# Kernel tuning notes

Measured on AMD Instinct MI355X. Metric: run time of the kernel, lower is better.

Reference implementation:

```python
import jax, jax.numpy as jnp
import numpy as np

B, C, W = 32768, 142, 10
K, D = 4096, 128
EPS = 1e-5


def _ln(x, g, b):
    m = jnp.mean(x, axis=-1, keepdims=True)
    v = jnp.var(x, axis=-1, keepdims=True)
    return (x - m) * jax.lax.rsqrt(v + EPS) * g + b


def setup_inputs() -> dict:
    key = jax.random.key(0)
    ks = jax.random.split(key, 10)
    s = lambda fi, fo: (2.0 / (fi + fo)) ** 0.5
    return {
        "x": jax.random.normal(ks[0], (B, C, W), jnp.float32),
        "W1": jax.random.normal(ks[1], (1420, 512), jnp.float32) * s(1420, 512),
        "b1": jnp.zeros((512,), jnp.float32),
        "g1": jnp.ones((512,), jnp.float32),
        "be1": jnp.zeros((512,), jnp.float32),
        "W2": jax.random.normal(ks[2], (512, 256), jnp.float32) * s(512, 256),
        "b2": jnp.zeros((256,), jnp.float32),
        "g2": jnp.ones((256,), jnp.float32),
        "be2": jnp.zeros((256,), jnp.float32),
        "W3": jax.random.normal(ks[3], (256, D), jnp.float32) * s(256, D),
        "b3": jnp.zeros((D,), jnp.float32),
        "emb": jax.random.normal(ks[4], (K, D), jnp.float32),
        "W4": jax.random.normal(ks[5], (D, 256), jnp.float32) * s(D, 256),
        "b4": jnp.zeros((256,), jnp.float32),
        "g3": jnp.ones((256,), jnp.float32),
        "be3": jnp.zeros((256,), jnp.float32),
        "W5": jax.random.normal(ks[6], (256, 128), jnp.float32) * s(256, 128),
        "b5": jnp.zeros((128,), jnp.float32),
        "W6": jax.random.normal(ks[7], (128, 2), jnp.float32) * s(128, 2),
        "b6": jnp.zeros((2,), jnp.float32),
    }


def reference(x, W1, b1, g1, be1, W2, b2, g2, be2, W3, b3, emb,
              W4, b4, g3, be3, W5, b5, W6, b6):
    # ----- encoder (eval mode: dropout is identity) -----
    xf = x.reshape(x.shape[0], -1)                      # [B, 1420]
    h = jax.nn.gelu(_ln(xf @ W1 + b1, g1, be1), approximate=False)
    h = jax.nn.gelu(_ln(h @ W2 + b2, g2, be2), approximate=False)
    z_e = h @ W3 + b3                                   # [B, D]

    # ----- EMA VQ (eval: no buffer updates) -----
    # squared distances give the same argmin as torch.cdist
    d2 = (jnp.sum(z_e * z_e, axis=-1, keepdims=True)
          - 2.0 * (z_e @ emb.T)
          + jnp.sum(emb * emb, axis=-1))                # [B, K]
    indices = jnp.argmin(d2, axis=-1)                   # [B] int
    z_q = emb[indices]                                  # [B, D]

    commitment_loss = 0.25 * jnp.mean((jax.lax.stop_gradient(z_q) - z_e) ** 2)
    z_q_st = z_e + jax.lax.stop_gradient(z_q - z_e)     # straight-through

    # histogram instead of materializing [B, K] one-hot
    counts = jnp.zeros((K,), jnp.float32).at[indices].add(1.0)
    avg_probs = counts / x.shape[0]
    perplexity = jnp.exp(-jnp.sum(avg_probs * jnp.log(avg_probs + 1e-10)))
    n_active = jnp.sum(avg_probs > 0.001)

    # ----- decoder (eval mode) -----
    d = jax.nn.gelu(_ln(z_q_st @ W4 + b4, g3, be3), approximate=False)
    d = jax.nn.gelu(d @ W5 + b5, approximate=False)
    velocity_pred = d @ W6 + b6                         # [B, 2]

    return (velocity_pred, z_e, z_q_st, indices, commitment_loss,
            perplexity, n_active)
```

## Files before the change

### kernel.cpp

```cpp
#include <hip/hip_runtime.h>

#define B_ROWS 32768
#define KCODES 4096

typedef float f32x4 __attribute__((ext_vector_type(4)));
typedef _Float16 f16x8 __attribute__((ext_vector_type(8)));
typedef _Float16 f16x4 __attribute__((ext_vector_type(4)));

struct Split { _Float16 h, m; };

__device__ __forceinline__ Split split2(float v)
{
  Split s;
  s.h = (_Float16)v;
  s.m = (_Float16)((v - (float)s.h) * 256.f);
  return s;
}

template<bool SPLITA>
__global__ __launch_bounds__(256, 3)
void hgemm(const float* __restrict__ Af, const _Float16* __restrict__ Ah,
           const _Float16* __restrict__ Am, int Astr,
           const _Float16* __restrict__ Bh, const _Float16* __restrict__ Bm,
           const float* __restrict__ bias, float* __restrict__ C,
           int M, int N, int K, int Kp, int nbx)
{
  __shared__ _Float16 As1[128 * 40];
  __shared__ _Float16 As2[128 * 40];
  __shared__ _Float16 Bs1[64 * 40];
  __shared__ _Float16 Bs2[64 * 40];

  const int flat = blockIdx.x;
  const int s_   = flat >> 3;
  const int mb   = (s_ / nbx) * 8 + (flat & 7);
  const int nb   = s_ % nbx;
  const int m0   = mb * 128;
  const int n0   = nb * 64;

  const int tid  = threadIdx.x;
  const int lane = tid & 63;
  const int wid  = tid >> 6;
  const int l15  = lane & 15;
  const int lg   = lane >> 4;
  const int wm   = (wid >> 1) * 64;
  const int wn   = (wid & 1) * 32;

  f32x4 hi[4][2], mid[4][2];
  #pragma unroll
  for (int i = 0; i < 4; ++i)
    #pragma unroll
    for (int j = 0; j < 2; ++j) { hi[i][j] = (f32x4)0.f; mid[i][j] = (f32x4)0.f; }

  const int sar = tid >> 1;
  const int sak = (tid & 1) << 4;
  const int far = tid >> 2;
  const int fak = (tid & 3) << 3;
  const int sbn = tid >> 2;
  const int sbk = (tid & 3) << 3;

  const int nk = Kp >> 5;
  #pragma unroll 1
  for (int kt = 0; kt < nk; ++kt) {
    const int k0 = kt << 5;
    if (SPLITA) {
      #pragma unroll
      for (int p = 0; p < 2; ++p) {
        const int r = far + (p << 6);
        const int c = k0 + fak;
        const float* src = Af + (size_t)(m0 + r) * K + c;
        float4 v0 = make_float4(0.f, 0.f, 0.f, 0.f), v1 = v0;
        if (c < K)     v0 = *reinterpret_cast<const float4*>(src);
        if (c + 4 < K) v1 = *reinterpret_cast<const float4*>(src + 4);
        const Split s0 = split2(v0.x), s1 = split2(v0.y), s2 = split2(v0.z), s3 = split2(v0.w);
        const Split s4 = split2(v1.x), s5 = split2(v1.y), s6 = split2(v1.z), s7 = split2(v1.w);
        f16x8 h, m;
        h[0]=s0.h; h[1]=s1.h; h[2]=s2.h; h[3]=s3.h; h[4]=s4.h; h[5]=s5.h; h[6]=s6.h; h[7]=s7.h;
        m[0]=s0.m; m[1]=s1.m; m[2]=s2.m; m[3]=s3.m; m[4]=s4.m; m[5]=s5.m; m[6]=s6.m; m[7]=s7.m;
        *reinterpret_cast<f16x8*>(&As1[r * 40 + fak]) = h;
        *reinterpret_cast<f16x8*>(&As2[r * 40 + fak]) = m;
      }
    } else {
      const size_t gA = (size_t)(m0 + sar) * Astr + k0 + sak;
      const int lA = sar * 40 + sak;
      *reinterpret_cast<uint4*>(&As1[lA])     = *reinterpret_cast<const uint4*>(Ah + gA);
      *reinterpret_cast<uint4*>(&As1[lA + 8]) = *reinterpret_cast<const uint4*>(Ah + gA + 8);
      *reinterpret_cast<uint4*>(&As2[lA])     = *reinterpret_cast<const uint4*>(Am + gA);
      *reinterpret_cast<uint4*>(&As2[lA + 8]) = *reinterpret_cast<const uint4*>(Am + gA + 8);
    }
    {
      const size_t gB = (size_t)(n0 + sbn) * Kp + k0 + sbk;
      const int lB = sbn * 40 + sbk;
      *reinterpret_cast<uint4*>(&Bs1[lB]) = *reinterpret_cast<const uint4*>(Bh + gB);
      *reinterpret_cast<uint4*>(&Bs2[lB]) = *reinterpret_cast<const uint4*>(Bm + gB);
    }
    __syncthreads();

    f16x8 a1[4], b[2];
    #pragma unroll
    for (int i = 0; i < 4; ++i)
      a1[i] = *reinterpret_cast<const f16x8*>(&As1[(wm + i * 16 + l15) * 40 + 8 * lg]);
    #pragma unroll
    for (int j = 0; j < 2; ++j)
      b[j] = *reinterpret_cast<const f16x8*>(&Bs1[(wn + j * 16 + l15) * 40 + 8 * lg]);
    #pragma unroll
    for (int i = 0; i < 4; ++i)
      #pragma unroll
      for (int j = 0; j < 2; ++j)
        hi[i][j] = __builtin_amdgcn_mfma_f32_16x16x32_f16(a1[i], b[j], hi[i][j], 0, 0, 0);
    #pragma unroll
    for (int i = 0; i < 4; ++i) {
      const f16x8 a2 = *reinterpret_cast<const f16x8*>(&As2[(wm + i * 16 + l15) * 40 + 8 * lg]);
      #pragma unroll
      for (int j = 0; j < 2; ++j)
        mid[i][j] = __builtin_amdgcn_mfma_f32_16x16x32_f16(a2, b[j], mid[i][j], 0, 0, 0);
    }
    #pragma unroll
    for (int j = 0; j < 2; ++j)
      b[j] = *reinterpret_cast<const f16x8*>(&Bs2[(wn + j * 16 + l15) * 40 + 8 * lg]);
    #pragma unroll
    for (int i = 0; i < 4; ++i)
      #pragma unroll
      for (int j = 0; j < 2; ++j)
        mid[i][j] = __builtin_amdgcn_mfma_f32_16x16x32_f16(a1[i], b[j], mid[i][j], 0, 0, 0);
    __syncthreads();
  }

  #pragma unroll
  for (int i = 0; i < 4; ++i)
    #pragma unroll
    for (int j = 0; j < 2; ++j) {
      const int col = n0 + wn + j * 16 + l15;
      const float bs = bias[col];
      #pragma unroll
      for (int r = 0; r < 4; ++r) {
        const int row = m0 + wm + i * 16 + 4 * lg + r;
        C[(size_t)row * N + col] = hi[i][j][r] + 0.00390625f * mid[i][j][r] + bs;
      }
    }
}

__global__ __launch_bounds__(256)
void ln_gelu_split(float* __restrict__ buf, const float* __restrict__ g,
                   const float* __restrict__ be, int Wd)
{
  __shared__ float rs[4], rs2[4];
  const int row = blockIdx.x;
  const int tid = threadIdx.x;
  float* x = buf + (size_t)row * Wd;
  const float v0 = x[tid];
  const float v1 = (Wd > 256) ? x[tid + 256] : 0.f;
  float s = v0 + v1, s2 = v0 * v0 + v1 * v1;
  #pragma unroll
  for (int m = 32; m; m >>= 1) { s += __shfl_down(s, m); s2 += __shfl_down(s2, m); }
  const int ln = tid & 63, wv = tid >> 6;
  if (ln == 0) { rs[wv] = s; rs2[wv] = s2; }
  __syncthreads();
  if (tid == 0) {
    const float S = rs[0] + rs[1] + rs[2] + rs[3];
    const float S2 = rs2[0] + rs2[1] + rs2[2] + rs2[3];
    const float mean = S / Wd;
    const float var = S2 / Wd - mean * mean;
    rs[0] = mean; rs2[0] = 1.0f / sqrtf(var + 1e-5f);
  }
  __syncthreads();
  const float mean = rs[0], inv = rs2[0];
  float y0 = (v0 - mean) * inv * g[tid] + be[tid];
  y0 = 0.5f * y0 * (1.f + erff(y0 * 0.70710678118654752f));
  float y1 = 0.f;
  if (Wd > 256) {
    y1 = (v1 - mean) * inv * g[tid + 256] + be[tid + 256];
    y1 = 0.5f * y1 * (1.f + erff(y1 * 0.70710678118654752f));
  }
  _Float16* hb = reinterpret_cast<_Float16*>(x);
  const Split s0 = split2(y0);
  hb[tid] = s0.h; hb[Wd + tid] = s0.m;
  if (Wd > 256) {
    const Split s1 = split2(y1);
    hb[tid + 256] = s1.h; hb[Wd + tid + 256] = s1.m;
  }
}

__global__ __launch_bounds__(256)
void vq_mfma(const float* __restrict__ Z, const _Float16* __restrict__ E1,
             const _Float16* __restrict__ E2, const float* __restrict__ e2,
             float* __restrict__ pval, int* __restrict__ pidx)
{
  __shared__ _Float16 Zs1[64 * 136];
  __shared__ _Float16 Zs2[64 * 136];
  __shared__ _Float16 Es1[128 * 40];
  __shared__ _Float16 Es2[128 * 40];

  const int flat = blockIdx.x;
  const int s_   = flat >> 3;
  const int mb   = (s_ >> 2) * 8 + (flat & 7);
  const int split = s_ & 3;
  const int m0   = mb * 64;

  const int tid  = threadIdx.x;
  const int lane = tid & 63;
  const int wid  = tid >> 6;
  const int l15  = lane & 15;
  const int lg   = lane >> 4;
  const int wn   = wid * 32;

  {
    const int zr = tid >> 2;
    #pragma unroll
    for (int q = 0; q < 8; ++q) {
      const int kk = ((tid & 3) << 2) + (q << 4);
      float4 v = *reinterpret_cast<const float4*>(Z + (size_t)(m0 + zr) * 128 + kk);
      const Split sx = split2(v.x), sy = split2(v.y), sz = split2(v.z), sw = split2(v.w);
      f16x4 h, m;
      h[0] = sx.h; h[1] = sy.h; h[2] = sz.h; h[3] = sw.h;
      m[0] = sx.m; m[1] = sy.m; m[2] = sz.m; m[3] = sw.m;
      *reinterpret_cast<f16x4*>(&Zs1[zr * 136 + kk]) = h;
      *reinterpret_cast<f16x4*>(&Zs2[zr * 136 + kk]) = m;
    }
  }

  float bv[16];
  int   bi[16];
  #pragma unroll
  for (int s = 0; s < 16; ++s) { bv[s] = 3.4e38f; bi[s] = 0x7fffffff; }

  const int sbn = tid >> 1;
  const int sbk = (tid & 1) << 4;

  #pragma unroll 1
  for (int ch = 0; ch < 8; ++ch) {
    const int n0 = split * 1024 + ch * 128;
    f32x4 hi[4][2], mid[4][2];
    #pragma unroll
    for (int i = 0; i < 4; ++i)
      #pragma unroll
      for (int j = 0; j < 2; ++j) { hi[i][j] = (f32x4)0.f; mid[i][j] = (f32x4)0.f; }

    #pragma unroll 1
    for (int kt = 0; kt < 4; ++kt) {
      const int k0 = kt << 5;
      {
        const size_t gb = (size_t)(n0 + sbn) * 128 + k0 + sbk;
        const int lb = sbn * 40 + sbk;
        *reinterpret_cast<uint4*>(&Es1[lb])     = *reinterpret_cast<const uint4*>(E1 + gb);
        *reinterpret_cast<uint4*>(&Es1[lb + 8]) = *reinterpret_cast<const uint4*>(E1 + gb + 8);
        *reinterpret_cast<uint4*>(&Es2[lb])     = *reinterpret_cast<const uint4*>(E2 + gb);
        *reinterpret_cast<uint4*>(&Es2[lb + 8]) = *reinterpret_cast<const uint4*>(E2 + gb + 8);
      }
      __syncthreads();

      f16x8 a[4], b[2], b2[2];
      #pragma unroll
      for (int i = 0; i < 4; ++i)
        a[i] = *reinterpret_cast<const f16x8*>(&Zs1[(i * 16 + l15) * 136 + k0 + 8 * lg]);
      #pragma unroll
      for (int j = 0; j < 2; ++j)
        b[j] = *reinterpret_cast<const f16x8*>(&Es1[(wn + j * 16 + l15) * 40 + 8 * lg]);
      #pragma unroll
      for (int i = 0; i < 4; ++i)
        #pragma unroll
        for (int j = 0; j < 2; ++j)
          hi[i][j] = __builtin_amdgcn_mfma_f32_16x16x32_f16(a[i], b[j], hi[i][j], 0, 0, 0);
      #pragma unroll
      for (int j = 0; j < 2; ++j)
        b2[j] = *reinterpret_cast<const f16x8*>(&Es2[(wn + j * 16 + l15) * 40 + 8 * lg]);
      #pragma unroll
      for (int i = 0; i < 4; ++i)
        #pragma unroll
        for (int j = 0; j < 2; ++j)
          mid[i][j] = __builtin_amdgcn_mfma_f32_16x16x32_f16(a[i], b2[j], mid[i][j], 0, 0, 0);
      #pragma unroll
      for (int i = 0; i < 4; ++i)
        a[i] = *reinterpret_cast<const f16x8*>(&Zs2[(i * 16 + l15) * 136 + k0 + 8 * lg]);
      #pragma unroll
      for (int i = 0; i < 4; ++i)
        #pragma unroll
        for (int j = 0; j < 2; ++j)
          mid[i][j] = __builtin_amdgcn_mfma_f32_16x16x32_f16(a[i], b[j], mid[i][j], 0, 0, 0);
      __syncthreads();
    }

    #pragma unroll
    for (int j = 0; j < 2; ++j) {
      const int c = n0 + wn + j * 16 + l15;
      const float ec = e2[c];
      #pragma unroll
      for (int i = 0; i < 4; ++i)
        #pragma unroll
        for (int r = 0; r < 4; ++r) {
          const float sc = ec - 2.f * (hi[i][j][r] + 0.00390625f * mid[i][j][r]);
          if (sc < bv[i * 4 + r]) { bv[i * 4 + r] = sc; bi[i * 4 + r] = c; }
        }
    }
  }

  #pragma unroll
  for (int s = 0; s < 16; ++s) {
    float v = bv[s]; int ix = bi[s];
    #pragma unroll
    for (int m = 1; m < 16; m <<= 1) {
      const float ov = __shfl_xor(v, m);
      const int   oi = __shfl_xor(ix, m);
      if (ov < v || (ov == v && oi < ix)) { v = ov; ix = oi; }
    }
    if (l15 == 0) {
      const int row = m0 + (s >> 2) * 16 + 4 * lg + (s & 3);
      pval[(size_t)row * 16 + split * 4 + wid] = v;
      pidx[(size_t)row * 16 + split * 4 + wid] = ix;
    }
  }
}

__global__ void prep_wT(const float* __restrict__ W, _Float16* __restrict__ Bh,
                        _Float16* __restrict__ Bm, int K, int N, int nshift,
                        int nmask, int Kp)
{
  const int i = blockIdx.x * 256 + threadIdx.x;
  if (i >= N * Kp) return;
  const int n = i & nmask;
  const int k = i >> nshift;
  const float v = (k < K) ? W[(size_t)k * N + n] : 0.f;
  const Split s = split2(v);
  Bh[(size_t)n * Kp + k] = s.h;
  Bm[(size_t)n * Kp + k] = s.m;
}

__global__ void prep_emb(const float* __restrict__ E, _Float16* __restrict__ E1,
                         _Float16* __restrict__ E2)
{
  const int i = blockIdx.x * 256 + threadIdx.x;
  const Split s = split2(E[i]);
  E1[i] = s.h; E2[i] = s.m;
}

__global__ void vq_reduce(const float* __restrict__ pval, const int* __restrict__ pidx,
                          int* __restrict__ idxout, float* __restrict__ idxf,
                          int* __restrict__ counts)
{
  const int b = blockIdx.x * 256 + threadIdx.x;
  if (b >= B_ROWS) return;
  float best = 3.4e38f; int bix = 0x7fffffff;
  #pragma unroll
  for (int j = 0; j < 16; ++j) {
    const float v = pval[(size_t)b * 16 + j];
    const int   ii = pidx[(size_t)b * 16 + j];
    if (v < best || (v == best && ii < bix)) { best = v; bix = ii; }
  }
  idxout[b] = bix;
  idxf[b] = (float)bix;
  atomicAdd(&counts[bix], 1);
}

__global__ __launch_bounds__(256)
void gather_commit(const int* __restrict__ idx, const float* __restrict__ E,
                   const float* __restrict__ ZE, float* __restrict__ ZQ,
                   float* __restrict__ cpart)
{
  __shared__ float red[4];
  const int b = blockIdx.x * 8 + (threadIdx.x >> 5);
  const int ch = threadIdx.x & 31;
  const int k = idx[b];
  float4 q = *reinterpret_cast<const float4*>(E + (size_t)k * 128 + ch * 4);
  float4 z = *reinterpret_cast<const float4*>(ZE + (size_t)b * 128 + ch * 4);
  *reinterpret_cast<float4*>(ZQ + (size_t)b * 128 + ch * 4) = q;
  float dx = q.x - z.x, dy = q.y - z.y, dz = q.z - z.z, dw = q.w - z.w;
  float s = dx * dx + dy * dy + dz * dz + dw * dw;
  #pragma unroll
  for (int m = 32; m; m >>= 1) s += __shfl_down(s, m);
  const int lane = threadIdx.x & 63, wv = threadIdx.x >> 6;
  if (lane == 0) red[wv] = s;
  __syncthreads();
  if (threadIdx.x == 0) cpart[blockIdx.x] = red[0] + red[1] + red[2] + red[3];
}

__global__ void e2_kernel(const float* __restrict__ E, float* __restrict__ e2)
{
  const int k = blockIdx.x * 256 + threadIdx.x;
  if (k >= KCODES) return;
  float s = 0.f;
  #pragma unroll 4
  for (int d = 0; d < 128; ++d) { float v = E[(size_t)k * 128 + d]; s += v * v; }
  e2[k] = s;
}

__global__ void zero_counts(int* counts)
{
  const int i = blockIdx.x * 256 + threadIdx.x;
  if (i < KCODES) counts[i] = 0;
}

__global__ void gelu_ew(float* __restrict__ p, int n)
{
  const int i = blockIdx.x * 256 + threadIdx.x;
  if (i < n) { float v = p[i]; p[i] = 0.5f * v * (1.f + erff(v * 0.70710678118654752f)); }
}

__global__ void gemm_n2(const float* __restrict__ T, const float* __restrict__ W6,
                        const float* __restrict__ b6, float* __restrict__ V, int M)
{
  const int r = blockIdx.x * 256 + threadIdx.x;
  if (r >= M) return;
  float a0 = b6[0], a1 = b6[1];
  #pragma unroll 4
  for (int d = 0; d < 128; ++d) {
    float t = T[(size_t)r * 128 + d];
    a0 = fmaf(t, W6[d * 2 + 0], a0);
    a1 = fmaf(t, W6[d * 2 + 1], a1);
  }
  V[r * 2 + 0] = a0; V[r * 2 + 1] = a1;
}

__global__ void vel_gather(const int* __restrict__ idx, const float* __restrict__ V,
                           float* __restrict__ out)
{
  const int b = blockIdx.x * 256 + threadIdx.x;
  if (b >= B_ROWS) return;
  const int k = idx[b];
  out[b * 2 + 0] = V[k * 2 + 0];
  out[b * 2 + 1] = V[k * 2 + 1];
}

__global__ __launch_bounds__(256)
void stats_kernel(const float* __restrict__ cpart, const int* __restrict__ counts,
                  float* __restrict__ outs)
{
  __shared__ float sh[256];
  __shared__ float sh2[256];
  __shared__ int shi[256];
  const int t = threadIdx.x;
  float cs = 0.f;
  for (int i = t; i < 4096; i += 256) cs += cpart[i];
  float h = 0.f; int act = 0;
  for (int k = t; k < KCODES; k += 256) {
    float avg = counts[k] * (1.0f / 32768.0f);
    h += avg * logf(avg + 1e-10f);
    act += (avg > 0.001f) ? 1 : 0;
  }
  sh[t] = cs; sh2[t] = h; shi[t] = act;
  __syncthreads();
  for (int s = 128; s; s >>= 1) {
    if (t < s) { sh[t] += sh[t + s]; sh2[t] += sh2[t + s]; shi[t] += shi[t + s]; }
    __syncthreads();
  }
  if (t == 0) {
    outs[0] = 0.25f * sh[0] / (32768.0f * 128.0f);
    outs[1] = expf(-sh2[0]);
    outs[2] = (float)shi[0];
  }
}

extern "C" void kernel_launch(void* const* d_in, const int* in_sizes, int n_in,
                              void* d_out, int out_size, void* d_ws, size_t ws_size,
                              hipStream_t stream)
{
  const float* x   = (const float*)d_in[0];
  const float* W1  = (const float*)d_in[1];
  const float* b1  = (const float*)d_in[2];
  const float* g1  = (const float*)d_in[3];
  const float* be1 = (const float*)d_in[4];
  const float* W2  = (const float*)d_in[5];
  const float* b2  = (const float*)d_in[6];
  const float* g2  = (const float*)d_in[7];
  const float* be2 = (const float*)d_in[8];
  const float* W3  = (const float*)d_in[9];
  const float* b3  = (const float*)d_in[10];
  const float* emb = (const float*)d_in[11];
  const float* W4  = (const float*)d_in[12];
  const float* b4  = (const float*)d_in[13];
  const float* g3  = (const float*)d_in[14];
  const float* be3 = (const float*)d_in[15];
  const float* W5  = (const float*)d_in[16];
  const float* b5  = (const float*)d_in[17];
  const float* W6  = (const float*)d_in[18];
  const float* b6  = (const float*)d_in[19];

  float* out = (float*)d_out;
  float* o_vel  = out;
  float* o_ze   = out + 65536;
  float* o_zq   = out + 65536 + B_ROWS * 128;
  float* o_idx  = out + 65536 + 2 * B_ROWS * 128;
  float* o_scal = o_idx + B_ROWS;

  float* ws = (float*)d_ws;
  float* h1f   = ws;
  float* pval  = ws;
  int*   pidx  = (int*)(ws + 524288);
  float* t1f   = ws + 1048576;
  float* t2    = ws + 2097152;
  float* vv    = ws + 2621440;
  float* h2f   = ws + 16777216;
  float* e2    = ws + 25165824;
  int*   ind   = (int*)(ws + 25169920);
  int*   cnt   = (int*)(ws + 25202688);
  float* cpart = ws + 25206784;
  _Float16* hb  = (_Float16*)(ws + 25210880);
  _Float16* E1  = hb;
  _Float16* E2  = E1 + 524288;
  _Float16* W1a = E2 + 524288;
  _Float16* W1b = W1a + 737280;
  _Float16* W2a = W1b + 737280;
  _Float16* W2b = W2a + 131072;
  _Float16* W3a = W2b + 131072;
  _Float16* W3b = W3a + 32768;
  _Float16* W4a = W3b + 32768;
  _Float16* W4b = W4a + 32768;
  _Float16* W5a = W4b + 32768;
  _Float16* W5b = W5a + 32768;

  zero_counts<<<16, 256, 0, stream>>>(cnt);
  e2_kernel<<<16, 256, 0, stream>>>(emb, e2);
  prep_emb<<<2048, 256, 0, stream>>>(emb, E1, E2);
  prep_wT<<<2880, 256, 0, stream>>>(W1, W1a, W1b, 1420, 512, 9, 511, 1440);
  prep_wT<<<512, 256, 0, stream>>>(W2, W2a, W2b, 512, 256, 8, 255, 512);
  prep_wT<<<128, 256, 0, stream>>>(W3, W3a, W3b, 256, 128, 7, 127, 256);
  prep_wT<<<128, 256, 0, stream>>>(W4, W4a, W4b, 128, 256, 8, 255, 128);
  prep_wT<<<128, 256, 0, stream>>>(W5, W5a, W5b, 256, 128, 7, 127, 256);

  hgemm<true><<<8 * 256, 256, 0, stream>>>(x, nullptr, nullptr, 0,
      W1a, W1b, b1, h1f, B_ROWS, 512, 1420, 1440, 8);
  ln_gelu_split<<<B_ROWS, 256, 0, stream>>>(h1f, g1, be1, 512);
  hgemm<false><<<4 * 256, 256, 0, stream>>>(nullptr,
      (const _Float16*)h1f, (const _Float16*)h1f + 512, 1024,
      W2a, W2b, b2, h2f, B_ROWS, 256, 512, 512, 4);
  ln_gelu_split<<<B_ROWS, 256, 0, stream>>>(h2f, g2, be2, 256);
  hgemm<false><<<2 * 256, 256, 0, stream>>>(nullptr,
      (const _Float16*)h2f, (const _Float16*)h2f + 256, 512,
      W3a, W3b, b3, o_ze, B_ROWS, 128, 256, 256, 2);

  vq_mfma<<<2048, 256, 0, stream>>>(o_ze, E1, E2, e2, pval, pidx);
  vq_reduce<<<128, 256, 0, stream>>>(pval, pidx, ind, o_idx, cnt);
  gather_commit<<<4096, 256, 0, stream>>>(ind, emb, o_ze, o_zq, cpart);

  hgemm<false><<<4 * 32, 256, 0, stream>>>(nullptr, E1, E2, 128,
      W4a, W4b, b4, t1f, KCODES, 256, 128, 128, 4);
  ln_gelu_split<<<KCODES, 256, 0, stream>>>(t1f, g3, be3, 256);
  hgemm<false><<<2 * 32, 256, 0, stream>>>(nullptr,
      (const _Float16*)t1f, (const _Float16*)t1f + 256, 512,
      W5a, W5b, b5, t2, KCODES, 128, 256, 256, 2);
  gelu_ew<<<(KCODES * 128 + 255) / 256, 256, 0, stream>>>(t2, KCODES * 128);
  gemm_n2<<<(KCODES + 255) / 256, 256, 0, stream>>>(t2, W6, b6, vv, KCODES);
  vel_gather<<<128, 256, 0, stream>>>(ind, vv, o_vel);

  stats_kernel<<<1, 256, 0, stream>>>(cpart, cnt, o_scal);
}
```

Before: 788.9 us.

## Load MFMA operands directly from global memory instead of staging through LDS

The GEMM kernels and the VQ distance kernel stop staging the B (weights/codebook) tiles, and for the smaller GEMMs also the A tiles, through shared memory. Each lane loads its MFMA fragments straight from global memory into registers. This removes LDS stores and reads and most of the __syncthreads barriers. The cost is redundant global/L2 traffic, since fragments are reread by several waves, plus partly strided loads that lose coalescing.

```diff
diff --git a/kernel.cpp b/kernel.cpp
--- a/kernel.cpp
+++ b/kernel.cpp
@@ -17,18 +17,14 @@
   return s;
 }
 
-template<bool SPLITA>
 __global__ __launch_bounds__(256, 3)
-void hgemm(const float* __restrict__ Af, const _Float16* __restrict__ Ah,
-           const _Float16* __restrict__ Am, int Astr,
-           const _Float16* __restrict__ Bh, const _Float16* __restrict__ Bm,
-           const float* __restrict__ bias, float* __restrict__ C,
-           int M, int N, int K, int Kp, int nbx)
+void hgemm1(const float* __restrict__ Af,
+            const _Float16* __restrict__ Bh, const _Float16* __restrict__ Bm,
+            const float* __restrict__ bias, float* __restrict__ C,
+            int M, int N, int K, int Kp, int nbx)
 {
   __shared__ _Float16 As1[128 * 40];
   __shared__ _Float16 As2[128 * 40];
-  __shared__ _Float16 Bs1[64 * 40];
-  __shared__ _Float16 Bs2[64 * 40];
 
   const int flat = blockIdx.x;
   const int s_   = flat >> 3;
@@ -51,78 +47,146 @@
     #pragma unroll
     for (int j = 0; j < 2; ++j) { hi[i][j] = (f32x4)0.f; mid[i][j] = (f32x4)0.f; }
 
-  const int sar = tid >> 1;
-  const int sak = (tid & 1) << 4;
   const int far = tid >> 2;
   const int fak = (tid & 3) << 3;
-  const int sbn = tid >> 2;
-  const int sbk = (tid & 3) << 3;
+
+  size_t boff[2];
+  #pragma unroll
+  for (int j = 0; j < 2; ++j)
+    boff[j] = (size_t)(n0 + wn + j * 16 + l15) * Kp + 8 * lg;
 
   const int nk = Kp >> 5;
   #pragma unroll 1
   for (int kt = 0; kt < nk; ++kt) {
     const int k0 = kt << 5;
-    if (SPLITA) {
-      #pragma unroll
-      for (int p = 0; p < 2; ++p) {
-        const int r = far + (p << 6);
-        const int c = k0 + fak;
-        const float* src = Af + (size_t)(m0 + r) * K + c;
-        float4 v0 = make_float4(0.f, 0.f, 0.f, 0.f), v1 = v0;
-        if (c < K)     v0 = *reinterpret_cast<const float4*>(src);
-        if (c + 4 < K) v1 = *reinterpret_cast<const float4*>(src + 4);
-        const Split s0 = split2(v0.x), s1 = split2(v0.y), s2 = split2(v0.z), s3 = split2(v0.w);
-        const Split s4 = split2(v1.x), s5 = split2(v1.y), s6 = split2(v1.z), s7 = split2(v1.w);
-        f16x8 h, m;
-        h[0]=s0.h; h[1]=s1.h; h[2]=s2.h; h[3]=s3.h; h[4]=s4.h; h[5]=s5.h; h[6]=s6.h; h[7]=s7.h;
-        m[0]=s0.m; m[1]=s1.m; m[2]=s2.m; m[3]=s3.m; m[4]=s4.m; m[5]=s5.m; m[6]=s6.m; m[7]=s7.m;
-        *reinterpret_cast<f16x8*>(&As1[r * 40 + fak]) = h;
-        *reinterpret_cast<f16x8*>(&As2[r * 40 + fak]) = m;
-      }
-    } else {
-      const size_t gA = (size_t)(m0 + sar) * Astr + k0 + sak;
-      const int lA = sar * 40 + sak;
-      *reinterpret_cast<uint4*>(&As1[lA])     = *reinterpret_cast<const uint4*>(Ah + gA);
-      *reinterpret_cast<uint4*>(&As1[lA + 8]) = *reinterpret_cast<const uint4*>(Ah + gA + 8);
-      *reinterpret_cast<uint4*>(&As2[lA])     = *reinterpret_cast<const uint4*>(Am + gA);
-      *reinterpret_cast<uint4*>(&As2[lA + 8]) = *reinterpret_cast<const uint4*>(Am + gA + 8);
-    }
-    {
-      const size_t gB = (size_t)(n0 + sbn) * Kp + k0 + sbk;
-      const int lB = sbn * 40 + sbk;
-      *reinterpret_cast<uint4*>(&Bs1[lB]) = *reinterpret_cast<const uint4*>(Bh + gB);
-      *reinterpret_cast<uint4*>(&Bs2[lB]) = *reinterpret_cast<const uint4*>(Bm + gB);
+    #pragma unroll
+    for (int p = 0; p < 2; ++p) {
+      const int r = far + (p << 6);
+      const int c = k0 + fak;
+      const float* src = Af + (size_t)(m0 + r) * K + c;
+      float4 v0 = make_float4(0.f, 0.f, 0.f, 0.f), v1 = v0;
+      if (c < K)     v0 = *reinterpret_cast<const float4*>(src);
+      if (c + 4 < K) v1 = *reinterpret_cast<const float4*>(src + 4);
+      const Split s0 = split2(v0.x), s1 = split2(v0.y), s2 = split2(v0.z), s3 = split2(v0.w);
+      const Split s4 = split2(v1.x), s5 = split2(v1.y), s6 = split2(v1.z), s7 = split2(v1.w);
+      f16x8 h, m;
+      h[0]=s0.h; h[1]=s1.h; h[2]=s2.h; h[3]=s3.h; h[4]=s4.h; h[5]=s5.h; h[6]=s6.h; h[7]=s7.h;
+      m[0]=s0.m; m[1]=s1.m; m[2]=s2.m; m[3]=s3.m; m[4]=s4.m; m[5]=s5.m; m[6]=s6.m; m[7]=s7.m;
+      *reinterpret_cast<f16x8*>(&As1[r * 40 + fak]) = h;
+      *reinterpret_cast<f16x8*>(&As2[r * 40 + fak]) = m;
+    }
+    f16x8 b1[2], b2[2];
+    #pragma unroll
+    for (int j = 0; j < 2; ++j) {
+      b1[j] = *reinterpret_cast<const f16x8*>(Bh + boff[j] + k0);
+      b2[j] = *reinterpret_cast<const f16x8*>(Bm + boff[j] + k0);
     }
     __syncthreads();
 
-    f16x8 a1[4], b[2];
+    f16x8 a1[4];
     #pragma unroll
     for (int i = 0; i < 4; ++i)
       a1[i] = *reinterpret_cast<const f16x8*>(&As1[(wm + i * 16 + l15) * 40 + 8 * lg]);
     #pragma unroll
-    for (int j = 0; j < 2; ++j)
-      b[j] = *reinterpret_cast<const f16x8*>(&Bs1[(wn + j * 16 + l15) * 40 + 8 * lg]);
-    #pragma unroll
     for (int i = 0; i < 4; ++i)
       #pragma unroll
       for (int j = 0; j < 2; ++j)
-        hi[i][j] = __builtin_amdgcn_mfma_f32_16x16x32_f16(a1[i], b[j], hi[i][j], 0, 0, 0);
+        hi[i][j] = __builtin_amdgcn_mfma_f32_16x16x32_f16(a1[i], b1[j], hi[i][j], 0, 0, 0);
     #pragma unroll
     for (int i = 0; i < 4; ++i) {
       const f16x8 a2 = *reinterpret_cast<const f16x8*>(&As2[(wm + i * 16 + l15) * 40 + 8 * lg]);
       #pragma unroll
       for (int j = 0; j < 2; ++j)
-        mid[i][j] = __builtin_amdgcn_mfma_f32_16x16x32_f16(a2, b[j], mid[i][j], 0, 0, 0);
-    }
-    #pragma unroll
-    for (int j = 0; j < 2; ++j)
-      b[j] = *reinterpret_cast<const f16x8*>(&Bs2[(wn + j * 16 + l15) * 40 + 8 * lg]);
+        mid[i][j] = __builtin_amdgcn_mfma_f32_16x16x32_f16(a2, b1[j], mid[i][j], 0, 0, 0);
+    }
     #pragma unroll
     for (int i = 0; i < 4; ++i)
       #pragma unroll
       for (int j = 0; j < 2; ++j)
-        mid[i][j] = __builtin_amdgcn_mfma_f32_16x16x32_f16(a1[i], b[j], mid[i][j], 0, 0, 0);
+        mid[i][j] = __builtin_amdgcn_mfma_f32_16x16x32_f16(a1[i], b2[j], mid[i][j], 0, 0, 0);
     __syncthreads();
+  }
+
+  #pragma unroll
+  for (int i = 0; i < 4; ++i)
+    #pragma unroll
+    for (int j = 0; j < 2; ++j) {
+      const int col = n0 + wn + j * 16 + l15;
+      const float bs = bias[col];
+      #pragma unroll
+      for (int r = 0; r < 4; ++r) {
+        const int row = m0 + wm + i * 16 + 4 * lg + r;
+        C[(size_t)row * N + col] = hi[i][j][r] + 0.00390625f * mid[i][j][r] + bs;
+      }
+    }
+}
+
+__global__ __launch_bounds__(256)
+void hgemm_reg(const _Float16* __restrict__ Ah, const _Float16* __restrict__ Am,
+               int Astr,
+               const _Float16* __restrict__ Bh, const _Float16* __restrict__ Bm,
+               const float* __restrict__ bias, float* __restrict__ C,
+               int N, int Kp, int nbx)
+{
+  const int flat = blockIdx.x;
+  const int s_   = flat >> 3;
+  const int mb   = (s_ / nbx) * 8 + (flat & 7);
+  const int nb   = s_ % nbx;
+  const int m0   = mb * 128;
+  const int n0   = nb * 64;
+
+  const int tid  = threadIdx.x;
+  const int lane = tid & 63;
+  const int wid  = tid >> 6;
+  const int l15  = lane & 15;
+  const int lg   = lane >> 4;
+  const int wm   = (wid >> 1) * 64;
+  const int wn   = (wid & 1) * 32;
+
+  f32x4 hi[4][2], mid[4][2];
+  #pragma unroll
+  for (int i = 0; i < 4; ++i)
+    #pragma unroll
+    for (int j = 0; j < 2; ++j) { hi[i][j] = (f32x4)0.f; mid[i][j] = (f32x4)0.f; }
+
+  size_t aoff[4], boff[2];
+  #pragma unroll
+  for (int i = 0; i < 4; ++i)
+    aoff[i] = (size_t)(m0 + wm + i * 16 + l15) * Astr + 8 * lg;
+  #pragma unroll
+  for (int j = 0; j < 2; ++j)
+    boff[j] = (size_t)(n0 + wn + j * 16 + l15) * Kp + 8 * lg;
+
+  const int nk = Kp >> 5;
+  #pragma unroll 1
+  for (int kt = 0; kt < nk; ++kt) {
+    const int k0 = kt << 5;
+    f16x8 a1[4], a2[4], b1[2], b2[2];
+    #pragma unroll
+    for (int i = 0; i < 4; ++i) {
+      a1[i] = *reinterpret_cast<const f16x8*>(Ah + aoff[i] + k0);
+      a2[i] = *reinterpret_cast<const f16x8*>(Am + aoff[i] + k0);
+    }
+    #pragma unroll
+    for (int j = 0; j < 2; ++j) {
+      b1[j] = *reinterpret_cast<const f16x8*>(Bh + boff[j] + k0);
+      b2[j] = *reinterpret_cast<const f16x8*>(Bm + boff[j] + k0);
+    }
+    #pragma unroll
+    for (int i = 0; i < 4; ++i)
+      #pragma unroll
+      for (int j = 0; j < 2; ++j)
+        hi[i][j] = __builtin_amdgcn_mfma_f32_16x16x32_f16(a1[i], b1[j], hi[i][j], 0, 0, 0);
+    #pragma unroll
+    for (int i = 0; i < 4; ++i)
+      #pragma unroll
+      for (int j = 0; j < 2; ++j)
+        mid[i][j] = __builtin_amdgcn_mfma_f32_16x16x32_f16(a2[i], b1[j], mid[i][j], 0, 0, 0);
+    #pragma unroll
+    for (int i = 0; i < 4; ++i)
+      #pragma unroll
+      for (int j = 0; j < 2; ++j)
+        mid[i][j] = __builtin_amdgcn_mfma_f32_16x16x32_f16(a1[i], b2[j], mid[i][j], 0, 0, 0);
   }
 
   #pragma unroll
@@ -187,8 +251,6 @@
 {
   __shared__ _Float16 Zs1[64 * 136];
   __shared__ _Float16 Zs2[64 * 136];
-  __shared__ _Float16 Es1[128 * 40];
-  __shared__ _Float16 Es2[128 * 40];
 
   const int flat = blockIdx.x;
   const int s_   = flat >> 3;
@@ -217,18 +279,21 @@
       *reinterpret_cast<f16x4*>(&Zs2[zr * 136 + kk]) = m;
     }
   }
+  __syncthreads();
 
   float bv[16];
   int   bi[16];
   #pragma unroll
   for (int s = 0; s < 16; ++s) { bv[s] = 3.4e38f; bi[s] = 0x7fffffff; }
-
-  const int sbn = tid >> 1;
-  const int sbk = (tid & 1) << 4;
 
   #pragma unroll 1
   for (int ch = 0; ch < 8; ++ch) {
     const int n0 = split * 1024 + ch * 128;
+    size_t eoff[2];
+    #pragma unroll
+    for (int j = 0; j < 2; ++j)
+      eoff[j] = (size_t)(n0 + wn + j * 16 + l15) * 128 + 8 * lg;
+
     f32x4 hi[4][2], mid[4][2];
     #pragma unroll
     for (int i = 0; i < 4; ++i)
@@ -238,45 +303,32 @@
     #pragma unroll 1
     for (int kt = 0; kt < 4; ++kt) {
       const int k0 = kt << 5;
-      {
-        const size_t gb = (size_t)(n0 + sbn) * 128 + k0 + sbk;
-        const int lb = sbn * 40 + sbk;
-        *reinterpret_cast<uint4*>(&Es1[lb])     = *reinterpret_cast<const uint4*>(E1 + gb);
-        *reinterpret_cast<uint4*>(&Es1[lb + 8]) = *reinterpret_cast<const uint4*>(E1 + gb + 8);
-        *reinterpret_cast<uint4*>(&Es2[lb])     = *reinterpret_cast<const uint4*>(E2 + gb);
-        *reinterpret_cast<uint4*>(&Es2[lb + 8]) = *reinterpret_cast<const uint4*>(E2 + gb + 8);
+      f16x8 a1[4], a2[4], b1[2], b2[2];
+      #pragma unroll
+      for (int i = 0; i < 4; ++i) {
+        a1[i] = *reinterpret_cast<const f16x8*>(&Zs1[(i * 16 + l15) * 136 + k0 + 8 * lg]);
+        a2[i] = *reinterpret_cast<const f16x8*>(&Zs2[(i * 16 + l15) * 136 + k0 + 8 * lg]);
       }
-      __syncthreads();
-
-      f16x8 a[4], b[2], b2[2];
-      #pragma unroll
-      for (int i = 0; i < 4; ++i)
-        a[i] = *reinterpret_cast<const f16x8*>(&Zs1[(i * 16 + l15) * 136 + k0 + 8 * lg]);
-      #pragma unroll
-      for (int j = 0; j < 2; ++j)
-        b[j] = *reinterpret_cast<const f16x8*>(&Es1[(wn + j * 16 + l15) * 40 + 8 * lg]);
+      #pragma unroll
+      for (int j = 0; j < 2; ++j) {
+        b1[j] = *reinterpret_cast<const f16x8*>(E1 + eoff[j] + k0);
+        b2[j] = *reinterpret_cast<const f16x8*>(E2 + eoff[j] + k0);
+      }
       #pragma unroll
       for (int i = 0; i < 4; ++i)
         #pragma unroll
         for (int j = 0; j < 2; ++j)
-          hi[i][j] = __builtin_amdgcn_mfma_f32_16x16x32_f16(a[i], b[j], hi[i][j], 0, 0, 0);
-      #pragma unroll
-      for (int j = 0; j < 2; ++j)
-        b2[j] = *reinterpret_cast<const f16x8*>(&Es2[(wn + j * 16 + l15) * 40 + 8 * lg]);
+          hi[i][j] = __builtin_amdgcn_mfma_f32_16x16x32_f16(a1[i], b1[j], hi[i][j], 0, 0, 0);
       #pragma unroll
       for (int i = 0; i < 4; ++i)
         #pragma unroll
         for (int j = 0; j < 2; ++j)
-          mid[i][j] = __builtin_amdgcn_mfma_f32_16x16x32_f16(a[i], b2[j], mid[i][j], 0, 0, 0);
-      #pragma unroll
-      for (int i = 0; i < 4; ++i)
-        a[i] = *reinterpret_cast<const f16x8*>(&Zs2[(i * 16 + l15) * 136 + k0 + 8 * lg]);
+          mid[i][j] = __builtin_amdgcn_mfma_f32_16x16x32_f16(a2[i], b1[j], mid[i][j], 0, 0, 0);
       #pragma unroll
       for (int i = 0; i < 4; ++i)
         #pragma unroll
         for (int j = 0; j < 2; ++j)
-          mid[i][j] = __builtin_amdgcn_mfma_f32_16x16x32_f16(a[i], b[j], mid[i][j], 0, 0, 0);
-      __syncthreads();
+          mid[i][j] = __builtin_amdgcn_mfma_f32_16x16x32_f16(a1[i], b2[j], mid[i][j], 0, 0, 0);
     }
 
     #pragma unroll
@@ -515,27 +567,24 @@
   prep_wT<<<128, 256, 0, stream>>>(W4, W4a, W4b, 128, 256, 8, 255, 128);
   prep_wT<<<128, 256, 0, stream>>>(W5, W5a, W5b, 256, 128, 7, 127, 256);
 
-  hgemm<true><<<8 * 256, 256, 0, stream>>>(x, nullptr, nullptr, 0,
-      W1a, W1b, b1, h1f, B_ROWS, 512, 1420, 1440, 8);
+  hgemm1<<<8 * 256, 256, 0, stream>>>(x, W1a, W1b, b1, h1f,
+                                      B_ROWS, 512, 1420, 1440, 8);
   ln_gelu_split<<<B_ROWS, 256, 0, stream>>>(h1f, g1, be1, 512);
-  hgemm<false><<<4 * 256, 256, 0, stream>>>(nullptr,
-      (const _Float16*)h1f, (const _Float16*)h1f + 512, 1024,
-      W2a, W2b, b2, h2f, B_ROWS, 256, 512, 512, 4);
+  hgemm_reg<<<4 * 256, 256, 0, stream>>>((const _Float16*)h1f,
+      (const _Float16*)h1f + 512, 1024, W2a, W2b, b2, h2f, 256, 512, 4);
   ln_gelu_split<<<B_ROWS, 256, 0, stream>>>(h2f, g2, be2, 256);
-  hgemm<false><<<2 * 256, 256, 0, stream>>>(nullptr,
-      (const _Float16*)h2f, (const _Float16*)h2f + 256, 512,
-      W3a, W3b, b3, o_ze, B_ROWS, 128, 256, 256, 2);
+  hgemm_reg<<<2 * 256, 256, 0, stream>>>((const _Float16*)h2f,
+      (const _Float16*)h2f + 256, 512, W3a, W3b, b3, o_ze, 128, 256, 2);
 
   vq_mfma<<<2048, 256, 0, stream>>>(o_ze, E1, E2, e2, pval, pidx);
   vq_reduce<<<128, 256, 0, stream>>>(pval, pidx, ind, o_idx, cnt);
   gather_commit<<<4096, 256, 0, stream>>>(ind, emb, o_ze, o_zq, cpart);
 
-  hgemm<false><<<4 * 32, 256, 0, stream>>>(nullptr, E1, E2, 128,
-      W4a, W4b, b4, t1f, KCODES, 256, 128, 128, 4);
+  hgemm_reg<<<4 * 32, 256, 0, stream>>>(E1, E2, 128,
+      W4a, W4b, b4, t1f, 256, 128, 4);
   ln_gelu_split<<<KCODES, 256, 0, stream>>>(t1f, g3, be3, 256);
-  hgemm<false><<<2 * 32, 256, 0, stream>>>(nullptr,
-      (const _Float16*)t1f, (const _Float16*)t1f + 256, 512,
-      W5a, W5b, b5, t2, KCODES, 128, 256, 256, 2);
+  hgemm_reg<<<2 * 32, 256, 0, stream>>>((const _Float16*)t1f,
+      (const _Float16*)t1f + 256, 512, W5a, W5b, b5, t2, 128, 256, 2);
   gelu_ew<<<(KCODES * 128 + 255) / 256, 256, 0, stream>>>(t2, KCODES * 128);
   gemm_n2<<<(KCODES + 255) / 256, 256, 0, stream>>>(t2, W6, b6, vv, KCODES);
   vel_gather<<<128, 256, 0, stream>>>(ind, vv, o_vel);
```

Result: slower. 921.6 us (+16.8%).

## Register-prefetch next K tile in GEMMs and VQ, optionally pre-split input x

Applied to the files above, without the earlier changes.

Adds register-level software prefetch to hgemm and vq_mfma: the next tile's global loads are issued right after the barrier, so they overlap with the MFMA work on the current tile. The VQ loop is flattened into a single loop over 32 tiles so prefetching can cross codebook-chunk boundaries. A prep_x kernel can also pre-split x into fp16 hi/mid buffers so the first GEMM avoids splitting in its inner loop, but it runs only when the workspace is large enough. The costs are more registers, which may lower occupancy, and extra memory traffic for the pre-split x.

```diff
diff --git a/kernel.cpp b/kernel.cpp
--- a/kernel.cpp
+++ b/kernel.cpp
@@ -51,28 +51,50 @@
     #pragma unroll
     for (int j = 0; j < 2; ++j) { hi[i][j] = (f32x4)0.f; mid[i][j] = (f32x4)0.f; }
 
+  const int far = tid >> 2;
+  const int fak = (tid & 3) << 3;
   const int sar = tid >> 1;
   const int sak = (tid & 1) << 4;
-  const int far = tid >> 2;
-  const int fak = (tid & 3) << 3;
   const int sbn = tid >> 2;
   const int sbk = (tid & 3) << 3;
 
-  const int nk = Kp >> 5;
-  #pragma unroll 1
-  for (int kt = 0; kt < nk; ++kt) {
-    const int k0 = kt << 5;
+  float4 va[2][2];
+  uint4 ra0, ra1, ra2, ra3;
+  uint4 rb0, rb1;
+
+  auto gload = [&](int k0) {
     if (SPLITA) {
       #pragma unroll
       for (int p = 0; p < 2; ++p) {
         const int r = far + (p << 6);
         const int c = k0 + fak;
         const float* src = Af + (size_t)(m0 + r) * K + c;
-        float4 v0 = make_float4(0.f, 0.f, 0.f, 0.f), v1 = v0;
-        if (c < K)     v0 = *reinterpret_cast<const float4*>(src);
-        if (c + 4 < K) v1 = *reinterpret_cast<const float4*>(src + 4);
-        const Split s0 = split2(v0.x), s1 = split2(v0.y), s2 = split2(v0.z), s3 = split2(v0.w);
-        const Split s4 = split2(v1.x), s5 = split2(v1.y), s6 = split2(v1.z), s7 = split2(v1.w);
+        va[p][0] = (c < K)     ? *reinterpret_cast<const float4*>(src)
+                               : make_float4(0.f, 0.f, 0.f, 0.f);
+        va[p][1] = (c + 4 < K) ? *reinterpret_cast<const float4*>(src + 4)
+                               : make_float4(0.f, 0.f, 0.f, 0.f);
+      }
+    } else {
+      const size_t gA = (size_t)(m0 + sar) * Astr + k0 + sak;
+      ra0 = *reinterpret_cast<const uint4*>(Ah + gA);
+      ra1 = *reinterpret_cast<const uint4*>(Ah + gA + 8);
+      ra2 = *reinterpret_cast<const uint4*>(Am + gA);
+      ra3 = *reinterpret_cast<const uint4*>(Am + gA + 8);
+    }
+    const size_t gB = (size_t)(n0 + sbn) * Kp + k0 + sbk;
+    rb0 = *reinterpret_cast<const uint4*>(Bh + gB);
+    rb1 = *reinterpret_cast<const uint4*>(Bm + gB);
+  };
+
+  auto lstore = [&]() {
+    if (SPLITA) {
+      #pragma unroll
+      for (int p = 0; p < 2; ++p) {
+        const int r = far + (p << 6);
+        const Split s0 = split2(va[p][0].x), s1 = split2(va[p][0].y),
+                    s2 = split2(va[p][0].z), s3 = split2(va[p][0].w);
+        const Split s4 = split2(va[p][1].x), s5 = split2(va[p][1].y),
+                    s6 = split2(va[p][1].z), s7 = split2(va[p][1].w);
         f16x8 h, m;
         h[0]=s0.h; h[1]=s1.h; h[2]=s2.h; h[3]=s3.h; h[4]=s4.h; h[5]=s5.h; h[6]=s6.h; h[7]=s7.h;
         m[0]=s0.m; m[1]=s1.m; m[2]=s2.m; m[3]=s3.m; m[4]=s4.m; m[5]=s5.m; m[6]=s6.m; m[7]=s7.m;
@@ -80,20 +102,24 @@
         *reinterpret_cast<f16x8*>(&As2[r * 40 + fak]) = m;
       }
     } else {
-      const size_t gA = (size_t)(m0 + sar) * Astr + k0 + sak;
       const int lA = sar * 40 + sak;
-      *reinterpret_cast<uint4*>(&As1[lA])     = *reinterpret_cast<const uint4*>(Ah + gA);
-      *reinterpret_cast<uint4*>(&As1[lA + 8]) = *reinterpret_cast<const uint4*>(Ah + gA + 8);
-      *reinterpret_cast<uint4*>(&As2[lA])     = *reinterpret_cast<const uint4*>(Am + gA);
-      *reinterpret_cast<uint4*>(&As2[lA + 8]) = *reinterpret_cast<const uint4*>(Am + gA + 8);
-    }
-    {
-      const size_t gB = (size_t)(n0 + sbn) * Kp + k0 + sbk;
-      const int lB = sbn * 40 + sbk;
-      *reinterpret_cast<uint4*>(&Bs1[lB]) = *reinterpret_cast<const uint4*>(Bh + gB);
-      *reinterpret_cast<uint4*>(&Bs2[lB]) = *reinterpret_cast<const uint4*>(Bm + gB);
-    }
+      *reinterpret_cast<uint4*>(&As1[lA])     = ra0;
+      *reinterpret_cast<uint4*>(&As1[lA + 8]) = ra1;
+      *reinterpret_cast<uint4*>(&As2[lA])     = ra2;
+      *reinterpret_cast<uint4*>(&As2[lA + 8]) = ra3;
+    }
+    const int lB = sbn * 40 + sbk;
+    *reinterpret_cast<uint4*>(&Bs1[lB]) = rb0;
+    *reinterpret_cast<uint4*>(&Bs2[lB]) = rb1;
+  };
+
+  const int nk = Kp >> 5;
+  gload(0);
+  #pragma unroll 1
+  for (int kt = 0; kt < nk; ++kt) {
+    lstore();
     __syncthreads();
+    if (kt + 1 < nk) gload((kt + 1) << 5);
 
     f16x8 a1[4], b[2];
     #pragma unroll
@@ -137,6 +163,23 @@
         C[(size_t)row * N + col] = hi[i][j][r] + 0.00390625f * mid[i][j][r] + bs;
       }
     }
+}
+
+__global__ __launch_bounds__(256)
+void prep_x(const float* __restrict__ x, _Float16* __restrict__ Xh,
+            _Float16* __restrict__ Xm)
+{
+  const size_t row = blockIdx.x;
+  #pragma unroll
+  for (int q = 0; q < 6; ++q) {
+    const int c = threadIdx.x + 256 * q;
+    if (c < 1440) {
+      const float v = (c < 1420) ? x[row * 1420 + c] : 0.f;
+      const Split s = split2(v);
+      Xh[row * 1440 + c] = s.h;
+      Xm[row * 1440 + c] = s.m;
+    }
+  }
 }
 
 __global__ __launch_bounds__(256)
@@ -225,72 +268,82 @@
 
   const int sbn = tid >> 1;
   const int sbk = (tid & 1) << 4;
-
+  const int lb  = sbn * 40 + sbk;
+
+  uint4 re0, re1, re2, re3;
+  auto eload = [&](int t) {
+    const int n0 = split * 1024 + (t >> 2) * 128;
+    const int k0 = (t & 3) << 5;
+    const size_t gb = (size_t)(n0 + sbn) * 128 + k0 + sbk;
+    re0 = *reinterpret_cast<const uint4*>(E1 + gb);
+    re1 = *reinterpret_cast<const uint4*>(E1 + gb + 8);
+    re2 = *reinterpret_cast<const uint4*>(E2 + gb);
+    re3 = *reinterpret_cast<const uint4*>(E2 + gb + 8);
+  };
+
+  f32x4 hi[4][2], mid[4][2];
+
+  eload(0);
   #pragma unroll 1
-  for (int ch = 0; ch < 8; ++ch) {
-    const int n0 = split * 1024 + ch * 128;
-    f32x4 hi[4][2], mid[4][2];
-    #pragma unroll
-    for (int i = 0; i < 4; ++i)
-      #pragma unroll
-      for (int j = 0; j < 2; ++j) { hi[i][j] = (f32x4)0.f; mid[i][j] = (f32x4)0.f; }
-
-    #pragma unroll 1
-    for (int kt = 0; kt < 4; ++kt) {
-      const int k0 = kt << 5;
-      {
-        const size_t gb = (size_t)(n0 + sbn) * 128 + k0 + sbk;
-        const int lb = sbn * 40 + sbk;
-        *reinterpret_cast<uint4*>(&Es1[lb])     = *reinterpret_cast<const uint4*>(E1 + gb);
-        *reinterpret_cast<uint4*>(&Es1[lb + 8]) = *reinterpret_cast<const uint4*>(E1 + gb + 8);
-        *reinterpret_cast<uint4*>(&Es2[lb])     = *reinterpret_cast<const uint4*>(E2 + gb);
-        *reinterpret_cast<uint4*>(&Es2[lb + 8]) = *reinterpret_cast<const uint4*>(E2 + gb + 8);
-      }
-      __syncthreads();
-
-      f16x8 a[4], b[2], b2[2];
-      #pragma unroll
-      for (int i = 0; i < 4; ++i)
-        a[i] = *reinterpret_cast<const f16x8*>(&Zs1[(i * 16 + l15) * 136 + k0 + 8 * lg]);
-      #pragma unroll
-      for (int j = 0; j < 2; ++j)
-        b[j] = *reinterpret_cast<const f16x8*>(&Es1[(wn + j * 16 + l15) * 40 + 8 * lg]);
+  for (int t = 0; t < 32; ++t) {
+    if ((t & 3) == 0) {
       #pragma unroll
       for (int i = 0; i < 4; ++i)
         #pragma unroll
-        for (int j = 0; j < 2; ++j)
-          hi[i][j] = __builtin_amdgcn_mfma_f32_16x16x32_f16(a[i], b[j], hi[i][j], 0, 0, 0);
+        for (int j = 0; j < 2; ++j) { hi[i][j] = (f32x4)0.f; mid[i][j] = (f32x4)0.f; }
+    }
+    *reinterpret_cast<uint4*>(&Es1[lb])     = re0;
+    *reinterpret_cast<uint4*>(&Es1[lb + 8]) = re1;
+    *reinterpret_cast<uint4*>(&Es2[lb])     = re2;
+    *reinterpret_cast<uint4*>(&Es2[lb + 8]) = re3;
+    __syncthreads();
+    if (t + 1 < 32) eload(t + 1);
+
+    const int k0 = (t & 3) << 5;
+    f16x8 a1[4], b[2];
+    #pragma unroll
+    for (int i = 0; i < 4; ++i)
+      a1[i] = *reinterpret_cast<const f16x8*>(&Zs1[(i * 16 + l15) * 136 + k0 + 8 * lg]);
+    #pragma unroll
+    for (int j = 0; j < 2; ++j)
+      b[j] = *reinterpret_cast<const f16x8*>(&Es1[(wn + j * 16 + l15) * 40 + 8 * lg]);
+    #pragma unroll
+    for (int i = 0; i < 4; ++i)
       #pragma unroll
       for (int j = 0; j < 2; ++j)
-        b2[j] = *reinterpret_cast<const f16x8*>(&Es2[(wn + j * 16 + l15) * 40 + 8 * lg]);
-      #pragma unroll
-      for (int i = 0; i < 4; ++i)
+        hi[i][j] = __builtin_amdgcn_mfma_f32_16x16x32_f16(a1[i], b[j], hi[i][j], 0, 0, 0);
+    #pragma unroll
+    for (int i = 0; i < 4; ++i) {
+      const f16x8 a2 = *reinterpret_cast<const f16x8*>(&Zs2[(i * 16 + l15) * 136 + k0 + 8 * lg]);
+      #pragma unroll
+      for (int j = 0; j < 2; ++j)
+        mid[i][j] = __builtin_amdgcn_mfma_f32_16x16x32_f16(a2, b[j], mid[i][j], 0, 0, 0);
+    }
+    #pragma unroll
+    for (int j = 0; j < 2; ++j)
+      b[j] = *reinterpret_cast<const f16x8*>(&Es2[(wn + j * 16 + l15) * 40 + 8 * lg]);
+    #pragma unroll
+    for (int i = 0; i < 4; ++i)
+      #pragma unroll
+      for (int j = 0; j < 2; ++j)
+        mid[i][j] = __builtin_amdgcn_mfma_f32_16x16x32_f16(a1[i], b[j], mid[i][j], 0, 0, 0);
+
+    if ((t & 3) == 3) {
+      const int n0 = split * 1024 + (t >> 2) * 128;
+      #pragma unroll
+      for (int j = 0; j < 2; ++j) {
+        const int c = n0 + wn + j * 16 + l15;
+        const float ec = e2[c];
         #pragma unroll
-        for (int j = 0; j < 2; ++j)
-          mid[i][j] = __builtin_amdgcn_mfma_f32_16x16x32_f16(a[i], b2[j], mid[i][j], 0, 0, 0);
-      #pragma unroll
-      for (int i = 0; i < 4; ++i)
-        a[i] = *reinterpret_cast<const f16x8*>(&Zs2[(i * 16 + l15) * 136 + k0 + 8 * lg]);
-      #pragma unroll
-      for (int i = 0; i < 4; ++i)
-        #pragma unroll
-        for (int j = 0; j < 2; ++j)
-          mid[i][j] = __builtin_amdgcn_mfma_f32_16x16x32_f16(a[i], b[j], mid[i][j], 0, 0, 0);
-      __syncthreads();
-    }
-
-    #pragma unroll
-    for (int j = 0; j < 2; ++j) {
-      const int c = n0 + wn + j * 16 + l15;
-      const float ec = e2[c];
-      #pragma unroll
-      for (int i = 0; i < 4; ++i)
-        #pragma unroll
-        for (int r = 0; r < 4; ++r) {
-          const float sc = ec - 2.f * (hi[i][j][r] + 0.00390625f * mid[i][j][r]);
-          if (sc < bv[i * 4 + r]) { bv[i * 4 + r] = sc; bi[i * 4 + r] = c; }
-        }
-    }
+        for (int i = 0; i < 4; ++i)
+          #pragma unroll
+          for (int r = 0; r < 4; ++r) {
+            const float sc = ec - 2.f * (hi[i][j][r] + 0.00390625f * mid[i][j][r]);
+            if (sc < bv[i * 4 + r]) { bv[i * 4 + r] = sc; bi[i * 4 + r] = c; }
+          }
+      }
+    }
+    __syncthreads();
   }
 
   #pragma unroll
@@ -506,6 +559,10 @@
   _Float16* W5a = W4b + 32768;
   _Float16* W5b = W5a + 32768;
 
+  _Float16* Xh = (_Float16*)(ws + 26701824);
+  _Float16* Xm = Xh + 47185920;
+  const bool presplit_x = ws_size >= (size_t)73887744 * 4;
+
   zero_counts<<<16, 256, 0, stream>>>(cnt);
   e2_kernel<<<16, 256, 0, stream>>>(emb, e2);
   prep_emb<<<2048, 256, 0, stream>>>(emb, E1, E2);
@@ -515,8 +572,14 @@
   prep_wT<<<128, 256, 0, stream>>>(W4, W4a, W4b, 128, 256, 8, 255, 128);
   prep_wT<<<128, 256, 0, stream>>>(W5, W5a, W5b, 256, 128, 7, 127, 256);
 
-  hgemm<true><<<8 * 256, 256, 0, stream>>>(x, nullptr, nullptr, 0,
-      W1a, W1b, b1, h1f, B_ROWS, 512, 1420, 1440, 8);
+  if (presplit_x) {
+    prep_x<<<B_ROWS, 256, 0, stream>>>(x, Xh, Xm);
+    hgemm<false><<<8 * 256, 256, 0, stream>>>(nullptr, Xh, Xm, 1440,
+        W1a, W1b, b1, h1f, B_ROWS, 512, 1440, 1440, 8);
+  } else {
+    hgemm<true><<<8 * 256, 256, 0, stream>>>(x, nullptr, nullptr, 0,
+        W1a, W1b, b1, h1f, B_ROWS, 512, 1420, 1440, 8);
+  }
   ln_gelu_split<<<B_ROWS, 256, 0, stream>>>(h1f, g1, be1, 512);
   hgemm<false><<<4 * 256, 256, 0, stream>>>(nullptr,
       (const _Float16*)h1f, (const _Float16*)h1f + 512, 1024,
```

Result: slower. 849.1 us (+7.6%).
